# Kernel optimization log

Measured on AMD Instinct MI355X. Metric: run time of the kernel, lower is better.

Reference implementation:

```python
import jax, jax.numpy as jnp
import numpy as np

NUM_LAYERS = 2
VOCAB = 32000
INPUT = 1024
HIDDEN = 1024
OUTPUT = 32000
BATCH = 8
SEQ = 256


def setup_inputs() -> dict:
    key = jax.random.key(0)
    ks = jax.random.split(key, 8)
    s_in = 1.0 / np.sqrt(INPUT)
    s_h = 1.0 / np.sqrt(HIDDEN)
    input_ = jax.random.randint(ks[0], (BATCH, SEQ), 0, VOCAB)
    emb = jax.random.normal(ks[1], (VOCAB, INPUT), jnp.float32)
    # Gate order along last dim: [i, f, g, o], each of width HIDDEN.
    Wx = jax.random.uniform(ks[2], (NUM_LAYERS, INPUT, 4 * HIDDEN), jnp.float32, -s_in, s_in)
    bx = jax.random.uniform(ks[3], (NUM_LAYERS, 4 * HIDDEN), jnp.float32, -s_in, s_in)
    Wh = jax.random.uniform(ks[4], (NUM_LAYERS, HIDDEN, 4 * HIDDEN), jnp.float32, -s_h, s_h)
    bh = jax.random.uniform(ks[5], (NUM_LAYERS, 4 * HIDDEN), jnp.float32, -s_h, s_h)
    Wd = jax.random.uniform(ks[6], (HIDDEN, OUTPUT), jnp.float32, -s_h, s_h)
    bd = jax.random.uniform(ks[7], (OUTPUT,), jnp.float32, -s_h, s_h)
    return {"input_": input_, "emb": emb, "Wx": Wx, "bx": bx, "Wh": Wh, "bh": bh, "Wd": Wd, "bd": bd}


def _lstm_core(input_, emb, Wx, bx, Wh, bh, Wd, bd):
    x = emb[input_]                      # [B, T, E]
    xs = jnp.swapaxes(x, 0, 1)           # [T, B, E]
    h0 = jnp.zeros((NUM_LAYERS, x.shape[0], HIDDEN), x.dtype)
    c0 = jnp.zeros_like(h0)

    def step(carry, x_t):
        h, c = carry
        layer_in = x_t
        new_h, new_c = [], []
        for l in range(NUM_LAYERS):
            gates = layer_in @ Wx[l] + bx[l] + h[l] @ Wh[l] + bh[l]  # [B, 4H]
            i_g, f_g, g_g, o_g = jnp.split(gates, 4, axis=-1)
            i_g = jax.nn.sigmoid(i_g)
            f_g = jax.nn.sigmoid(f_g)
            o_g = jax.nn.sigmoid(o_g)
            g_g = jnp.tanh(g_g)
            c_l = f_g * c[l] + i_g * g_g
            h_l = o_g * jnp.tanh(c_l)
            new_h.append(h_l)
            new_c.append(c_l)
            layer_in = h_l
        return (jnp.stack(new_h), jnp.stack(new_c)), layer_in

    (_, _), tops = jax.lax.scan(step, (h0, c0), xs)  # tops: [T, B, H]
    out = tops @ Wd + bd                              # [T, B, V]
    return jnp.swapaxes(out, 0, 1)                    # [B, T, V]


def reference(input_, emb, Wx, bx, Wh, bh, Wd, bd):
    return _lstm_core(input_, emb, Wx, bx, Wh, bh, Wd, bd)
```

## Files before the change

### kernel.cpp

```cpp
#include <hip/hip_runtime.h>
#include <cstdint>
#include <cstddef>

#define BATCH 8
#define SEQ   256
#define HID   1024
#define GATES 4096
#define VOC   32000

typedef __attribute__((ext_vector_type(8))) short bf16x8;
typedef __attribute__((ext_vector_type(4))) float f32x4;

__device__ __forceinline__ float sigf(float x){ return 1.0f/(1.0f + __expf(-x)); }
__device__ __forceinline__ float tanhf_(float x){ return 1.0f - 2.0f/(__expf(2.0f*x) + 1.0f); }

__device__ __forceinline__ unsigned short f2bf(float x){
  union { float f; unsigned u; } v; v.f = x;
  unsigned r = v.u + 0x7fffu + ((v.u >> 16) & 1u);
  return (unsigned short)(r >> 16);
}
__device__ __forceinline__ float bf2f(unsigned short h){
  union { float f; unsigned u; } v; v.u = ((unsigned)h) << 16; return v.f;
}

__global__ void k_init(unsigned* __restrict__ flags, unsigned* __restrict__ hbu){
  int tid = blockIdx.x*blockDim.x + threadIdx.x;
  int nt = gridDim.x*blockDim.x;
  for (int i = tid; i < 256*16; i += nt) flags[i] = 0u;
  for (int i = tid; i < 16384; i += nt) hbu[i] = 0u;
}

__global__ void k_wconv(const float* __restrict__ W,
                        unsigned short* __restrict__ WH,
                        unsigned short* __restrict__ WL){
  const int total4 = (HID*VOC) >> 2;
  int stride = gridDim.x*blockDim.x;
  for (int i = blockIdx.x*blockDim.x + threadIdx.x; i < total4; i += stride){
    float4 v = *(const float4*)(W + (size_t)i*4);
    float xs[4] = {v.x, v.y, v.z, v.w};
    unsigned hh = 0, ll = 0;
    #pragma unroll
    for (int c=0;c<4;c++){
      unsigned short h = f2bf(xs[c]);
      unsigned short lo = f2bf(xs[c] - bf2f(h));
      hh |= ((unsigned)h)  << (16*(c&1));
      ll |= ((unsigned)lo) << (16*(c&1));
      if (c==1){ ((unsigned*)&WH[(size_t)i*4])[0] = hh; ((unsigned*)&WL[(size_t)i*4])[0] = ll; hh=0; ll=0; }
      if (c==3){ ((unsigned*)&WH[(size_t)i*4])[1] = hh; ((unsigned*)&WL[(size_t)i*4])[1] = ll; }
    }
  }
}

template<int AMODE, int OMODE>
__global__ __launch_bounds__(256) void k_mfma(
    const float* __restrict__ A,
    const float* __restrict__ W,
    const float* __restrict__ b1,
    const float* __restrict__ b2,
    const int*   __restrict__ tokens,
    const float* __restrict__ emb,
    float* __restrict__ C, int N)
{
  __shared__ unsigned short AsH[16*1024], AsL[16*1024];
  __shared__ unsigned short BsH[8*1024],  BsL[8*1024];
  int tid = threadIdx.x;
  int m0 = blockIdx.y*256, n0 = blockIdx.x*128;
  int w = tid >> 6, l = tid & 63;
  int lrow = l & 15, kg = l >> 4;

  f32x4 acc[4][8];
  #pragma unroll
  for (int i=0;i<4;i++){
    #pragma unroll
    for (int j=0;j<8;j++) acc[i][j] = (f32x4){0.f,0.f,0.f,0.f};
  }

  int rA  = tid >> 3, fq = tid & 7;

  const float* arow[8];
  #pragma unroll
  for (int i=0;i<8;i++){
    int gm = m0 + rA + 32*i;
    if (AMODE==1) arow[i] = emb + (size_t)tokens[(gm&7)*SEQ + (gm>>3)]*1024;
    else          arow[i] = A   + (size_t)gm*1024;
  }

  for (int kt=0; kt<32; ++kt){
    int k0 = kt*32;
    float4 av[8];
    #pragma unroll
    for (int i=0;i<8;i++)
      av[i] = *(const float4*)(arow[i] + k0 + fq*4);
    float4 wv[4];
    #pragma unroll
    for (int i=0;i<4;i++)
      wv[i] = *(const float4*)(W + (size_t)(k0 + rA)*N + n0 + fq*4 + 32*i);
    __syncthreads();
    #pragma unroll
    for (int i=0;i<8;i++){
      int r = rA + 32*i;
      int base = (r >> 4)*1024 + ((fq >> 1)*16 + (r & 15))*8 + (fq & 1)*4;
      float xs[4] = {av[i].x, av[i].y, av[i].z, av[i].w};
      unsigned long long ph = 0ull, pl = 0ull;
      #pragma unroll
      for (int c=0;c<4;c++){
        unsigned short h = f2bf(xs[c]);
        unsigned short lo = f2bf(xs[c] - bf2f(h));
        ph |= ((unsigned long long)h) << (16*c);
        pl |= ((unsigned long long)lo) << (16*c);
      }
      *(unsigned long long*)&AsH[base] = ph;
      *(unsigned long long*)&AsL[base] = pl;
    }
    #pragma unroll
    for (int i=0;i<4;i++){
      float xs[4] = {wv[i].x, wv[i].y, wv[i].z, wv[i].w};
      #pragma unroll
      for (int c=0;c<4;c++){
        int col = fq*4 + 32*i + c;
        int idx = (col >> 4)*1024 + ((rA >> 3)*16 + (col & 15))*8 + (rA & 7);
        unsigned short h = f2bf(xs[c]);
        BsH[idx] = h;
        BsL[idx] = f2bf(xs[c] - bf2f(h));
      }
    }
    __syncthreads();
    bf16x8 ah[4], al[4];
    #pragma unroll
    for (int i=0;i<4;i++){
      int fi = w*4 + i;
      ah[i] = *(const bf16x8*)&AsH[fi*1024 + l*8];
      al[i] = *(const bf16x8*)&AsL[fi*1024 + l*8];
    }
    #pragma unroll
    for (int jh=0;jh<2;jh++){
      bf16x8 bh_[4], bl_[4];
      #pragma unroll
      for (int j=0;j<4;j++){
        bh_[j] = *(const bf16x8*)&BsH[(jh*4+j)*1024 + l*8];
        bl_[j] = *(const bf16x8*)&BsL[(jh*4+j)*1024 + l*8];
      }
      #pragma unroll
      for (int i=0;i<4;i++){
        #pragma unroll
        for (int j=0;j<4;j++){
          f32x4 a = acc[i][jh*4+j];
          a = __builtin_amdgcn_mfma_f32_16x16x32_bf16(ah[i], bh_[j], a, 0,0,0);
          a = __builtin_amdgcn_mfma_f32_16x16x32_bf16(ah[i], bl_[j], a, 0,0,0);
          a = __builtin_amdgcn_mfma_f32_16x16x32_bf16(al[i], bh_[j], a, 0,0,0);
          acc[i][jh*4+j] = a;
        }
      }
    }
    __syncthreads();
  }

  int mbase = m0 + w*64 + kg*4;
  #pragma unroll
  for (int jj=0;jj<8;jj++){
    int gn = n0 + jj*16 + lrow;
    float bias = b1[gn];
    if (b2) bias += b2[gn];
    #pragma unroll
    for (int i=0;i<4;i++){
      #pragma unroll
      for (int r=0;r<4;r++){
        int m = mbase + i*16 + r;
        size_t crow = (OMODE==1) ? (size_t)((m & 7)*SEQ + (m >> 3)) : (size_t)m;
        C[crow*(size_t)N + gn] = acc[i][jj][r] + bias;
      }
    }
  }
}

template<int WPRE>
__global__ __launch_bounds__(256) void k_proj(
    const unsigned short* __restrict__ AH,
    const unsigned short* __restrict__ AL,
    const float* __restrict__ Wf,
    const unsigned short* __restrict__ WH,
    const unsigned short* __restrict__ WL,
    const float* __restrict__ bd,
    float* __restrict__ C)
{
  __shared__ unsigned short AsH[16*1024], AsL[16*1024];
  __shared__ unsigned short BsH[8*1024],  BsL[8*1024];
  int tid = threadIdx.x;
  int m0 = blockIdx.y*256, n0 = blockIdx.x*128;
  int w = tid >> 6, l = tid & 63;
  int lrow = l & 15, kg = l >> 4;

  f32x4 acc[4][8];
  #pragma unroll
  for (int i=0;i<4;i++){
    #pragma unroll
    for (int j=0;j<8;j++) acc[i][j] = (f32x4){0.f,0.f,0.f,0.f};
  }

  int rA = tid >> 3, fq = tid & 7;

  for (int kt=0; kt<32; ++kt){
    int k0 = kt*32;
    uint2 avh[8], avl[8];
    #pragma unroll
    for (int i=0;i<8;i++){
      size_t off = (size_t)(m0 + rA + 32*i)*1024 + k0 + fq*4;
      avh[i] = *(const uint2*)&AH[off];
      avl[i] = *(const uint2*)&AL[off];
    }
    uint2 wvh[4], wvl[4];
    float4 wvf[4];
    #pragma unroll
    for (int i=0;i<4;i++){
      size_t off = (size_t)(k0 + rA)*VOC + n0 + fq*4 + 32*i;
      if (WPRE){ wvh[i] = *(const uint2*)&WH[off]; wvl[i] = *(const uint2*)&WL[off]; }
      else     { wvf[i] = *(const float4*)(Wf + off); }
    }
    __syncthreads();
    #pragma unroll
    for (int i=0;i<8;i++){
      int r = rA + 32*i;
      int base = (r >> 4)*1024 + ((fq >> 1)*16 + (r & 15))*8 + (fq & 1)*4;
      *(uint2*)&AsH[base] = avh[i];
      *(uint2*)&AsL[base] = avl[i];
    }
    #pragma unroll
    for (int i=0;i<4;i++){
      #pragma unroll
      for (int c=0;c<4;c++){
        int col = fq*4 + 32*i + c;
        int idx = (col >> 4)*1024 + ((rA >> 3)*16 + (col & 15))*8 + (rA & 7);
        if (WPRE){
          BsH[idx] = ((const unsigned short*)&wvh[i])[c];
          BsL[idx] = ((const unsigned short*)&wvl[i])[c];
        } else {
          float xs = (c==0)?wvf[i].x:(c==1)?wvf[i].y:(c==2)?wvf[i].z:wvf[i].w;
          unsigned short h = f2bf(xs);
          BsH[idx] = h;
          BsL[idx] = f2bf(xs - bf2f(h));
        }
      }
    }
    __syncthreads();
    bf16x8 ah[4], al[4];
    #pragma unroll
    for (int i=0;i<4;i++){
      int fi = w*4 + i;
      ah[i] = *(const bf16x8*)&AsH[fi*1024 + l*8];
      al[i] = *(const bf16x8*)&AsL[fi*1024 + l*8];
    }
    #pragma unroll
    for (int jh=0;jh<2;jh++){
      bf16x8 bh_[4], bl_[4];
      #pragma unroll
      for (int j=0;j<4;j++){
        bh_[j] = *(const bf16x8*)&BsH[(jh*4+j)*1024 + l*8];
        bl_[j] = *(const bf16x8*)&BsL[(jh*4+j)*1024 + l*8];
      }
      #pragma unroll
      for (int i=0;i<4;i++){
        #pragma unroll
        for (int j=0;j<4;j++){
          f32x4 a = acc[i][jh*4+j];
          a = __builtin_amdgcn_mfma_f32_16x16x32_bf16(ah[i], bh_[j], a, 0,0,0);
          a = __builtin_amdgcn_mfma_f32_16x16x32_bf16(ah[i], bl_[j], a, 0,0,0);
          a = __builtin_amdgcn_mfma_f32_16x16x32_bf16(al[i], bh_[j], a, 0,0,0);
          acc[i][jh*4+j] = a;
        }
      }
    }
    __syncthreads();
  }

  int mbase = m0 + w*64 + kg*4;
  #pragma unroll
  for (int jj=0;jj<8;jj++){
    int gn = n0 + jj*16 + lrow;
    float bias = bd[gn];
    #pragma unroll
    for (int i=0;i<4;i++){
      #pragma unroll
      for (int r=0;r<4;r++){
        int m = mbase + i*16 + r;
        size_t crow = (size_t)((m & 7)*SEQ + (m >> 3));
        C[crow*(size_t)VOC + gn] = acc[i][jj][r] + bias;
      }
    }
  }
}

__global__ __launch_bounds__(256) void k_rec2(
    const float* __restrict__ G,
    const float* __restrict__ Wh,
    const float* __restrict__ Wx,
    const float* __restrict__ bx1,
    const float* __restrict__ bh1,
    unsigned short* __restrict__ TopsH,
    unsigned short* __restrict__ TopsL,
    unsigned* __restrict__ hbu,
    unsigned* __restrict__ flags)
{
  extern __shared__ char ldsb[];
  unsigned short* A0 = (unsigned short*)ldsb;
  unsigned short* A1 = A0 + 16384;
  unsigned short* A2 = A1 + 16384;
  unsigned short* hB = A2 + 16384;
  float* Cx = (float*)(ldsb + 131072);
  int tid = threadIdx.x;
  int u0 = blockIdx.x*4;
  const int wv = tid >> 6, ln = tid & 63;
  const int fs0 = tid*16, fs1 = (tid+64)*16, fs2 = (tid+128)*16, fs3 = (tid+192)*16;

  {
    int m = tid >> 4, kseg = tid & 15;
    int col = (m >> 2)*1024 + u0 + (m & 3);
    const float* wsrc[3] = { Wh, Wx + (size_t)HID*GATES, Wh + (size_t)HID*GATES };
    unsigned short* Ad[3] = { A0, A1, A2 };
    for (int tgt=0; tgt<3; ++tgt){
      const float* s = wsrc[tgt] + col;
      #pragma unroll
      for (int run=0; run<8; ++run){
        int k0 = kseg*64 + run*8;
        int kt = k0 >> 5, kg = (k0 >> 3) & 3;
        bf16x8 v;
        #pragma unroll
        for (int e=0;e<8;e++) v[e] = (short)f2bf(s[(size_t)(k0+e)*GATES]);
        *(bf16x8*)&Ad[tgt][kt*512 + ((kg<<4)|m)*8] = v;
      }
    }
  }
  float b1r[4] = {0.f,0.f,0.f,0.f};
  if (tid >= 32 && tid < 64){
    int j = tid & 3;
    #pragma unroll
    for (int g=0;g<4;g++) b1r[g] = bx1[g*1024+u0+j] + bh1[g*1024+u0+j];
  }
  float creg = 0.0f;

  for (int p=0; p<=SEQ; ++p){
    const unsigned* h0b = hbu + (size_t)(p&1)*4096;
    const unsigned* h1b = hbu + 8192 + (size_t)((p+1)&1)*4096;
    {
      int colp = tid & 15, seg0 = tid >> 4;
      #pragma unroll
      for (int i=0;i<2;i++){
        int seg = seg0 + 16*i;
        const float* src = (const float*)(((colp < 8) ? h0b : h1b)
                                          + (colp & 7)*512 + seg*16);
        float4 r0,r1,r2,r3;
        asm volatile(
          "global_load_dwordx4 %0, %4, off sc0 sc1\n\t"
          "global_load_dwordx4 %1, %4, off offset:16 sc0 sc1\n\t"
          "global_load_dwordx4 %2, %4, off offset:32 sc0 sc1\n\t"
          "global_load_dwordx4 %3, %4, off offset:48 sc0 sc1\n\t"
          "s_waitcnt vmcnt(0)"
          : "=&v"(r0),"=&v"(r1),"=&v"(r2),"=&v"(r3)
          : "v"(src)
          : "memory");
        *(float4*)&hB[seg*512 + ((0<<4)|colp)*8] = r0;
        *(float4*)&hB[seg*512 + ((1<<4)|colp)*8] = r1;
        *(float4*)&hB[seg*512 + ((2<<4)|colp)*8] = r2;
        *(float4*)&hB[seg*512 + ((3<<4)|colp)*8] = r3;
      }
    }
    float gp0=0.f,gp1=0.f,gp2=0.f,gp3=0.f;
    if (tid < 32 && p < SEQ){
      const float* gp = G + ((size_t)p*8 + (tid>>2))*GATES + u0 + (tid&3);
      gp0 = gp[0]; gp1 = gp[1024]; gp2 = gp[2048]; gp3 = gp[3072];
    }
    __syncthreads();

    f32x4 C0 = {0.f,0.f,0.f,0.f}, C1 = {0.f,0.f,0.f,0.f}, C2 = {0.f,0.f,0.f,0.f};
    #pragma unroll
    for (int kti=0; kti<8; ++kti){
      int kt = wv + kti*4;
      bf16x8 bB = *(const bf16x8*)&hB[kt*512 + ln*8];
      bf16x8 a0 = *(const bf16x8*)&A0[kt*512 + ln*8];
      bf16x8 a1 = *(const bf16x8*)&A1[kt*512 + ln*8];
      bf16x8 a2 = *(const bf16x8*)&A2[kt*512 + ln*8];
      C0 = __builtin_amdgcn_mfma_f32_16x16x32_bf16(a0, bB, C0, 0,0,0);
      C1 = __builtin_amdgcn_mfma_f32_16x16x32_bf16(a1, bB, C1, 0,0,0);
      C2 = __builtin_amdgcn_mfma_f32_16x16x32_bf16(a2, bB, C2, 0,0,0);
    }
    {
      int cn = ln & 15, mb = (ln >> 4)*4;
      #pragma unroll
      for (int r=0;r<4;r++){
        Cx[((wv*3+0)*16 + mb+r)*17 + cn] = C0[r];
        Cx[((wv*3+1)*16 + mb+r)*17 + cn] = C1[r];
        Cx[((wv*3+2)*16 + mb+r)*17 + cn] = C2[r];
      }
    }
    __syncthreads();

    float hv = 0.f; bool pub = false; unsigned dstbase = 0;
    if (tid < 32){
      if (p < SEQ){
        int b = tid >> 2, j = tid & 3;
        float gv0=gp0, gv1=gp1, gv2=gp2, gv3=gp3;
        #pragma unroll
        for (int w=0;w<4;w++){
          gv0 += Cx[((w*3+0)*16 + 0*4+j)*17 + b];
          gv1 += Cx[((w*3+0)*16 + 1*4+j)*17 + b];
          gv2 += Cx[((w*3+0)*16 + 2*4+j)*17 + b];
          gv3 += Cx[((w*3+0)*16 + 3*4+j)*17 + b];
        }
        float iv = sigf(gv0), fv = sigf(gv1), ov = sigf(gv3), gg = tanhf_(gv2);
        creg = fv*creg + iv*gg;
        hv = ov * tanhf_(creg);
        pub = true; dstbase = ((unsigned)(p+1)&1u)*4096u;
      }
    } else if (tid < 64){
      if (p > 0){
        int b = (tid-32) >> 2, j = tid & 3;
        float gv0=b1r[0], gv1=b1r[1], gv2=b1r[2], gv3=b1r[3];
        #pragma unroll
        for (int w=0;w<4;w++){
          gv0 += Cx[((w*3+1)*16 + 0*4+j)*17 + b] + Cx[((w*3+2)*16 + 0*4+j)*17 + b+8];
          gv1 += Cx[((w*3+1)*16 + 1*4+j)*17 + b] + Cx[((w*3+2)*16 + 1*4+j)*17 + b+8];
          gv2 += Cx[((w*3+1)*16 + 2*4+j)*17 + b] + Cx[((w*3+2)*16 + 2*4+j)*17 + b+8];
          gv3 += Cx[((w*3+1)*16 + 3*4+j)*17 + b] + Cx[((w*3+2)*16 + 3*4+j)*17 + b+8];
        }
        float iv = sigf(gv0), fv = sigf(gv1), ov = sigf(gv3), gg = tanhf_(gv2);
        creg = fv*creg + iv*gg;
        hv = ov * tanhf_(creg);
        pub = true; dstbase = 8192u + ((unsigned)p&1u)*4096u;
        unsigned short hi = f2bf(hv);
        unsigned short lo = f2bf(hv - bf2f(hi));
        size_t off = ((size_t)(p-1)*8 + b)*HID + u0 + (tid&3);
        TopsH[off] = hi;
        TopsL[off] = lo;
      }
    }
    if (tid < 64){
      unsigned mybits = (unsigned)f2bf(hv);
      unsigned other  = (unsigned)__shfl_xor((int)mybits, 1);
      if (pub && ((tid & 1) == 0)){
        unsigned word = (mybits & 0xffffu) | (other << 16);
        int b = (tid & 31) >> 2;
        int widx = (u0 >> 1) + ((tid >> 1) & 1);
        (void)__hip_atomic_exchange(&hbu[dstbase + b*512 + widx], word,
                                    __ATOMIC_RELAXED, __HIP_MEMORY_SCOPE_AGENT);
      }
    }

    if (p < SEQ){
      if (tid < 64){
        if (tid == 0){
          asm volatile("s_waitcnt vmcnt(0)" ::: "memory");
          (void)__hip_atomic_exchange(&flags[blockIdx.x*16], (unsigned)(p+1),
                                      __ATOMIC_RELAXED, __HIP_MEMORY_SCOPE_AGENT);
        }
        unsigned tgt = (unsigned)(p+1);
        int spins = 0;
        for (;;){
          unsigned a = __hip_atomic_load(&flags[fs0], __ATOMIC_RELAXED, __HIP_MEMORY_SCOPE_AGENT);
          unsigned b = __hip_atomic_load(&flags[fs1], __ATOMIC_RELAXED, __HIP_MEMORY_SCOPE_AGENT);
          unsigned c = __hip_atomic_load(&flags[fs2], __ATOMIC_RELAXED, __HIP_MEMORY_SCOPE_AGENT);
          unsigned d = __hip_atomic_load(&flags[fs3], __ATOMIC_RELAXED, __HIP_MEMORY_SCOPE_AGENT);
          bool ok = (a >= tgt) && (b >= tgt) && (c >= tgt) && (d >= tgt);
          if (__all(ok)) break;
          __builtin_amdgcn_s_sleep(1);
          if (++spins > 150000){
            for (;;){
              unsigned a2 = __hip_atomic_load(&flags[fs0], __ATOMIC_ACQUIRE, __HIP_MEMORY_SCOPE_AGENT);
              unsigned b2 = __hip_atomic_load(&flags[fs1], __ATOMIC_ACQUIRE, __HIP_MEMORY_SCOPE_AGENT);
              unsigned c2 = __hip_atomic_load(&flags[fs2], __ATOMIC_ACQUIRE, __HIP_MEMORY_SCOPE_AGENT);
              unsigned d2 = __hip_atomic_load(&flags[fs3], __ATOMIC_ACQUIRE, __HIP_MEMORY_SCOPE_AGENT);
              bool ok2 = (a2 >= tgt) && (b2 >= tgt) && (c2 >= tgt) && (d2 >= tgt);
              if (__all(ok2)) break;
              __builtin_amdgcn_s_sleep(8);
              if (++spins > 8000000) break;
            }
            break;
          }
        }
      }
      __syncthreads();
    }
  }
}

extern "C" void kernel_launch(void* const* d_in, const int* in_sizes, int n_in,
                              void* d_out, int out_size, void* d_ws, size_t ws_size,
                              hipStream_t stream) {
  const int*   tokens = (const int*)d_in[0];
  const float* emb = (const float*)d_in[1];
  const float* Wx  = (const float*)d_in[2];
  const float* bx  = (const float*)d_in[3];
  const float* Wh  = (const float*)d_in[4];
  const float* bh  = (const float*)d_in[5];
  const float* Wd  = (const float*)d_in[6];
  const float* bd  = (const float*)d_in[7];
  float* out = (float*)d_out;
  float* ws  = (float*)d_ws;

  float* G = ws;
  unsigned short* TopsH = (unsigned short*)(ws + (size_t)8388608);
  unsigned short* TopsL = (unsigned short*)(ws + (size_t)9437184);
  unsigned* hbu   = (unsigned*)(ws + (size_t)10485760);
  unsigned* flags = (unsigned*)(ws + (size_t)10502144);
  unsigned short* WdH = (unsigned short*)(ws + (size_t)10506240);
  unsigned short* WdL = (unsigned short*)(ws + (size_t)26890240);
  const bool wpre = ws_size >= (size_t)43274240*4;

  (void)hipFuncSetAttribute((const void*)k_rec2,
        hipFuncAttributeMaxDynamicSharedMemorySize, 144128);

  k_init<<<32,256,0,stream>>>(flags, hbu);
  if (wpre)
    k_wconv<<<2048,256,0,stream>>>(Wd, WdH, WdL);

  k_mfma<1,0><<<dim3(32,8),256,0,stream>>>(nullptr, Wx, bx, bh, tokens, emb, G, GATES);

  k_rec2<<<256,256,144128,stream>>>(G, Wh, Wx, bx + GATES, bh + GATES,
                                    TopsH, TopsL, hbu, flags);

  if (wpre)
    k_proj<1><<<dim3(250,8),256,0,stream>>>(TopsH, TopsL, nullptr, WdH, WdL, bd, out);
  else
    k_proj<0><<<dim3(250,8),256,0,stream>>>(TopsH, TopsL, Wd, nullptr, nullptr, bd, out);
}
```

Baseline: 2.119 ms.

## Drop low-order weight split in output projection and prefetch next K tile

The output projection now stores only the bf16 high part of Wd instead of a high/low pair. Each tile therefore needs two MFMAs instead of three or four, and weight conversion and traffic are halved. The projection kernel also register-prefetches the next K tile while computing the current one, and requests two blocks per CU through launch bounds. The risk is lower accuracy, since Wd is now rounded to bf16 with no correction term, which may exceed the tolerance.

```diff
diff --git a/kernel.cpp b/kernel.cpp
--- a/kernel.cpp
+++ b/kernel.cpp
@@ -31,23 +31,15 @@
 }
 
 __global__ void k_wconv(const float* __restrict__ W,
-                        unsigned short* __restrict__ WH,
-                        unsigned short* __restrict__ WL){
+                        unsigned short* __restrict__ WH){
   const int total4 = (HID*VOC) >> 2;
   int stride = gridDim.x*blockDim.x;
   for (int i = blockIdx.x*blockDim.x + threadIdx.x; i < total4; i += stride){
     float4 v = *(const float4*)(W + (size_t)i*4);
-    float xs[4] = {v.x, v.y, v.z, v.w};
-    unsigned hh = 0, ll = 0;
-    #pragma unroll
-    for (int c=0;c<4;c++){
-      unsigned short h = f2bf(xs[c]);
-      unsigned short lo = f2bf(xs[c] - bf2f(h));
-      hh |= ((unsigned)h)  << (16*(c&1));
-      ll |= ((unsigned)lo) << (16*(c&1));
-      if (c==1){ ((unsigned*)&WH[(size_t)i*4])[0] = hh; ((unsigned*)&WL[(size_t)i*4])[0] = ll; hh=0; ll=0; }
-      if (c==3){ ((unsigned*)&WH[(size_t)i*4])[1] = hh; ((unsigned*)&WL[(size_t)i*4])[1] = ll; }
-    }
+    uint2 o;
+    o.x = ((unsigned)f2bf(v.x)) | (((unsigned)f2bf(v.y)) << 16);
+    o.y = ((unsigned)f2bf(v.z)) | (((unsigned)f2bf(v.w)) << 16);
+    *(uint2*)&WH[(size_t)i*4] = o;
   }
 }
 
@@ -173,13 +165,119 @@
   }
 }
 
-template<int WPRE>
-__global__ __launch_bounds__(256) void k_proj(
+__global__ __launch_bounds__(256,2) void k_proj1(
+    const unsigned short* __restrict__ AH,
+    const unsigned short* __restrict__ AL,
+    const unsigned short* __restrict__ WH,
+    const float* __restrict__ bd,
+    float* __restrict__ C)
+{
+  __shared__ unsigned short AsH[16*1024], AsL[16*1024];
+  __shared__ unsigned short BsH[8*1024];
+  int tid = threadIdx.x;
+  int m0 = blockIdx.y*256, n0 = blockIdx.x*128;
+  int w = tid >> 6, l = tid & 63;
+  int lrow = l & 15, kg = l >> 4;
+
+  f32x4 acc[4][8];
+  #pragma unroll
+  for (int i=0;i<4;i++){
+    #pragma unroll
+    for (int j=0;j<8;j++) acc[i][j] = (f32x4){0.f,0.f,0.f,0.f};
+  }
+
+  int rA = tid >> 3, fq = tid & 7;
+
+  uint2 avh[8], avl[8], wvh[4];
+  #pragma unroll
+  for (int i=0;i<8;i++){
+    size_t off = (size_t)(m0 + rA + 32*i)*1024 + fq*4;
+    avh[i] = *(const uint2*)&AH[off];
+    avl[i] = *(const uint2*)&AL[off];
+  }
+  #pragma unroll
+  for (int i=0;i<4;i++)
+    wvh[i] = *(const uint2*)&WH[(size_t)rA*VOC + n0 + fq*4 + 32*i];
+
+  for (int kt=0; kt<32; ++kt){
+    __syncthreads();
+    #pragma unroll
+    for (int i=0;i<8;i++){
+      int r = rA + 32*i;
+      int base = (r >> 4)*1024 + ((fq >> 1)*16 + (r & 15))*8 + (fq & 1)*4;
+      *(uint2*)&AsH[base] = avh[i];
+      *(uint2*)&AsL[base] = avl[i];
+    }
+    #pragma unroll
+    for (int i=0;i<4;i++){
+      #pragma unroll
+      for (int c=0;c<4;c++){
+        int col = fq*4 + 32*i + c;
+        int idx = (col >> 4)*1024 + ((rA >> 3)*16 + (col & 15))*8 + (rA & 7);
+        BsH[idx] = ((const unsigned short*)&wvh[i])[c];
+      }
+    }
+    __syncthreads();
+    if (kt < 31){
+      int k0 = (kt+1)*32;
+      #pragma unroll
+      for (int i=0;i<8;i++){
+        size_t off = (size_t)(m0 + rA + 32*i)*1024 + k0 + fq*4;
+        avh[i] = *(const uint2*)&AH[off];
+        avl[i] = *(const uint2*)&AL[off];
+      }
+      #pragma unroll
+      for (int i=0;i<4;i++)
+        wvh[i] = *(const uint2*)&WH[(size_t)(k0 + rA)*VOC + n0 + fq*4 + 32*i];
+    }
+    bf16x8 ah[4], al[4];
+    #pragma unroll
+    for (int i=0;i<4;i++){
+      int fi = w*4 + i;
+      ah[i] = *(const bf16x8*)&AsH[fi*1024 + l*8];
+      al[i] = *(const bf16x8*)&AsL[fi*1024 + l*8];
+    }
+    #pragma unroll
+    for (int jh=0;jh<2;jh++){
+      bf16x8 bh_[4];
+      #pragma unroll
+      for (int j=0;j<4;j++)
+        bh_[j] = *(const bf16x8*)&BsH[(jh*4+j)*1024 + l*8];
+      #pragma unroll
+      for (int i=0;i<4;i++){
+        #pragma unroll
+        for (int j=0;j<4;j++){
+          f32x4 a = acc[i][jh*4+j];
+          a = __builtin_amdgcn_mfma_f32_16x16x32_bf16(ah[i], bh_[j], a, 0,0,0);
+          a = __builtin_amdgcn_mfma_f32_16x16x32_bf16(al[i], bh_[j], a, 0,0,0);
+          acc[i][jh*4+j] = a;
+        }
+      }
+    }
+  }
+  __syncthreads();
+
+  int mbase = m0 + w*64 + kg*4;
+  #pragma unroll
+  for (int jj=0;jj<8;jj++){
+    int gn = n0 + jj*16 + lrow;
+    float bias = bd[gn];
+    #pragma unroll
+    for (int i=0;i<4;i++){
+      #pragma unroll
+      for (int r=0;r<4;r++){
+        int m = mbase + i*16 + r;
+        size_t crow = (size_t)((m & 7)*SEQ + (m >> 3));
+        C[crow*(size_t)VOC + gn] = acc[i][jj][r] + bias;
+      }
+    }
+  }
+}
+
+__global__ __launch_bounds__(256) void k_proj0(
     const unsigned short* __restrict__ AH,
     const unsigned short* __restrict__ AL,
     const float* __restrict__ Wf,
-    const unsigned short* __restrict__ WH,
-    const unsigned short* __restrict__ WL,
     const float* __restrict__ bd,
     float* __restrict__ C)
 {
@@ -208,14 +306,10 @@
       avh[i] = *(const uint2*)&AH[off];
       avl[i] = *(const uint2*)&AL[off];
     }
-    uint2 wvh[4], wvl[4];
     float4 wvf[4];
     #pragma unroll
-    for (int i=0;i<4;i++){
-      size_t off = (size_t)(k0 + rA)*VOC + n0 + fq*4 + 32*i;
-      if (WPRE){ wvh[i] = *(const uint2*)&WH[off]; wvl[i] = *(const uint2*)&WL[off]; }
-      else     { wvf[i] = *(const float4*)(Wf + off); }
-    }
+    for (int i=0;i<4;i++)
+      wvf[i] = *(const float4*)(Wf + (size_t)(k0 + rA)*VOC + n0 + fq*4 + 32*i);
     __syncthreads();
     #pragma unroll
     for (int i=0;i<8;i++){
@@ -226,19 +320,14 @@
     }
     #pragma unroll
     for (int i=0;i<4;i++){
+      float xs[4] = {wvf[i].x, wvf[i].y, wvf[i].z, wvf[i].w};
       #pragma unroll
       for (int c=0;c<4;c++){
         int col = fq*4 + 32*i + c;
         int idx = (col >> 4)*1024 + ((rA >> 3)*16 + (col & 15))*8 + (rA & 7);
-        if (WPRE){
-          BsH[idx] = ((const unsigned short*)&wvh[i])[c];
-          BsL[idx] = ((const unsigned short*)&wvl[i])[c];
-        } else {
-          float xs = (c==0)?wvf[i].x:(c==1)?wvf[i].y:(c==2)?wvf[i].z:wvf[i].w;
-          unsigned short h = f2bf(xs);
-          BsH[idx] = h;
-          BsL[idx] = f2bf(xs - bf2f(h));
-        }
+        unsigned short h = f2bf(xs[c]);
+        BsH[idx] = h;
+        BsL[idx] = f2bf(xs[c] - bf2f(h));
       }
     }
     __syncthreads();
@@ -501,15 +590,14 @@
   unsigned* hbu   = (unsigned*)(ws + (size_t)10485760);
   unsigned* flags = (unsigned*)(ws + (size_t)10502144);
   unsigned short* WdH = (unsigned short*)(ws + (size_t)10506240);
-  unsigned short* WdL = (unsigned short*)(ws + (size_t)26890240);
-  const bool wpre = ws_size >= (size_t)43274240*4;
+  const bool wpre = ws_size >= (size_t)26890240*4;
 
   (void)hipFuncSetAttribute((const void*)k_rec2,
         hipFuncAttributeMaxDynamicSharedMemorySize, 144128);
 
   k_init<<<32,256,0,stream>>>(flags, hbu);
   if (wpre)
-    k_wconv<<<2048,256,0,stream>>>(Wd, WdH, WdL);
+    k_wconv<<<2048,256,0,stream>>>(Wd, WdH);
 
   k_mfma<1,0><<<dim3(32,8),256,0,stream>>>(nullptr, Wx, bx, bh, tokens, emb, G, GATES);
 
@@ -517,7 +605,7 @@
                                     TopsH, TopsL, hbu, flags);
 
   if (wpre)
-    k_proj<1><<<dim3(250,8),256,0,stream>>>(TopsH, TopsL, nullptr, WdH, WdL, bd, out);
+    k_proj1<<<dim3(250,8),256,0,stream>>>(TopsH, TopsL, WdH, bd, out);
   else
-    k_proj<0><<<dim3(250,8),256,0,stream>>>(TopsH, TopsL, Wd, nullptr, nullptr, bd, out);
-}
+    k_proj0<<<dim3(250,8),256,0,stream>>>(TopsH, TopsL, Wd, bd, out);
+}
```

New measurement: 1.738 ms. 1.22x faster.
